# Performance work log

Measured on AMD Instinct MI355X. Metric: run time of the kernel, lower is better.

Reference implementation:

```python
import jax, jax.numpy as jnp
import numpy as np
import math

B, S, D, L, H, V, MAXP = 8, 512, 1024, 6, 8, 32000, 4096
HD = D // H
FF = 4 * D
EPS = 1e-5
SCALE = 1.0 / math.sqrt(HD)


def _ln(x, g, b):
    m = x.mean(-1, keepdims=True)
    xm = x - m
    v = (xm * xm).mean(-1, keepdims=True)
    return xm * jax.lax.rsqrt(v + EPS) * g + b


def setup_inputs() -> dict:
    key = jax.random.key(0)
    ks = jax.random.split(key, 16)
    std = 0.02
    inp = {
        'input_ids': jax.random.randint(ks[0], (B, S), 0, V, dtype=jnp.int32),
        'attention_mask': jnp.ones((B, S), dtype=jnp.int32),
        'current_position': 0,
        'tok_emb': jax.random.normal(ks[1], (V, D), jnp.float32) * std,
        'pos_emb': jax.random.normal(ks[2], (MAXP, D), jnp.float32) * std,
        'ln1_s': jnp.ones((L, D), jnp.float32),
        'ln1_b': jnp.zeros((L, D), jnp.float32),
        'Wq': jax.random.normal(ks[3], (L, D, D), jnp.float32) * std,
        'bq': jnp.zeros((L, D), jnp.float32),
        'Wk': jax.random.normal(ks[4], (L, D, D), jnp.float32) * std,
        'bk': jnp.zeros((L, D), jnp.float32),
        'Wv': jax.random.normal(ks[5], (L, D, D), jnp.float32) * std,
        'bv': jnp.zeros((L, D), jnp.float32),
        'Wo': jax.random.normal(ks[6], (L, D, D), jnp.float32) * std,
        'bo': jnp.zeros((L, D), jnp.float32),
        'ln2_s': jnp.ones((L, D), jnp.float32),
        'ln2_b': jnp.zeros((L, D), jnp.float32),
        'W1': jax.random.normal(ks[7], (L, D, FF), jnp.float32) * std,
        'b1': jnp.zeros((L, FF), jnp.float32),
        'W2': jax.random.normal(ks[8], (L, FF, D), jnp.float32) * std,
        'b2': jnp.zeros((L, D), jnp.float32),
        'lnf_s': jnp.ones((D,), jnp.float32),
        'lnf_b': jnp.zeros((D,), jnp.float32),
        'Wout': jax.random.normal(ks[9], (D, D), jnp.float32) * std,
        'bout': jnp.zeros((D,), jnp.float32),
    }
    return inp


def reference(input_ids, attention_mask, current_position, tok_emb, pos_emb,
              ln1_s, ln1_b, Wq, bq, Wk, bk, Wv, bv, Wo, bo,
              ln2_s, ln2_b, W1, b1, W2, b2, lnf_s, lnf_b, Wout, bout):
    pos = current_position + jnp.arange(S)  # [S]
    h = tok_emb[input_ids] + pos_emb[pos][None, :, :]  # [B,S,D]
    pad = (attention_mask == 0)[:, None, None, :]  # [B,1,1,S] key-padding mask

    def layer(h, p):
        (l1s, l1b, wq, bq_, wk, bk_, wv, bv_, wo, bo_,
         l2s, l2b, w1, b1_, w2, b2_) = p
        x = _ln(h, l1s, l1b)
        q = (x @ wq + bq_).reshape(B, S, H, HD).transpose(0, 2, 1, 3)
        k = (x @ wk + bk_).reshape(B, S, H, HD).transpose(0, 2, 1, 3)
        v = (x @ wv + bv_).reshape(B, S, H, HD).transpose(0, 2, 1, 3)
        scores = jnp.einsum('bhqd,bhkd->bhqk', q, k) * SCALE
        scores = jnp.where(pad, -10000.0, scores)
        attn = jax.nn.softmax(scores, axis=-1)
        o = jnp.einsum('bhqk,bhkd->bhqd', attn, v)
        o = o.transpose(0, 2, 1, 3).reshape(B, S, D)
        h = h + (o @ wo + bo_)
        x = _ln(h, l2s, l2b)
        mlp = jax.nn.gelu(x @ w1 + b1_, approximate=False) @ w2 + b2_
        return h + mlp, None

    h, _ = jax.lax.scan(layer, h, (ln1_s, ln1_b, Wq, bq, Wk, bk, Wv, bv, Wo, bo,
                                   ln2_s, ln2_b, W1, b1, W2, b2))
    h = _ln(h, lnf_s, lnf_b)
    return h @ Wout + bout
```

## Files before the change

### kernel.cpp

```cpp
#include <hip/hip_runtime.h>
#include <hip/hip_bf16.h>
#include <math.h>

#define BB 8
#define SS 512
#define DD 1024
#define LL 6
#define HH 8
#define HDD 128
#define FFF 4096
#define EPSF 1e-5f
#define SCALEF 0.08838834764831845f

typedef __attribute__((ext_vector_type(8))) _Float16 f16x8;
typedef __attribute__((ext_vector_type(4))) _Float16 f16x4;
typedef __attribute__((ext_vector_type(4))) float f32x4;

__device__ __forceinline__ void gload16(const void* g, void* l) {
  __builtin_amdgcn_global_load_lds(
      (const __attribute__((address_space(1))) void*)g,
      (__attribute__((address_space(3))) void*)l, 16, 0, 0);
}

__global__ __launch_bounds__(256, 3) void gemmk_kernel(
    const _Float16* __restrict__ Ag, const _Float16* __restrict__ Bg,
    const float* __restrict__ bias, void* __restrict__ outp,
    const int* __restrict__ amask, int Ndim, int Kdim, int Kstr,
    long zsA, long zsB, long zsOut, int emode) {
  __shared__ _Float16 lA[8192];
  __shared__ _Float16 lB[8192];
  const int tid = threadIdx.x;
  const int lane = tid & 63;
  const int wid = tid >> 6;
  const int z = blockIdx.z;
  const int m0 = blockIdx.y * 128;
  const int n0 = blockIdx.x * 128;
  const long K2 = (long)Kstr * 2;
  const _Float16* Az = Ag + (long)z * zsA + (long)m0 * Kstr;
  const _Float16* Bz = Bg + (long)z * zsB + (long)n0 * Kstr;

  const int wm = (wid >> 1) * 64;
  const int wn = (wid & 1) * 64;
  const int r16 = lane & 15;
  const int kq = lane >> 4;

  const char* As[4];
  const char* Bs[4];
  int ldd[4];
#pragma unroll
  for (int i = 0; i < 4; ++i) {
    const int idx = tid + i * 256;
    const int r = idx >> 3;
    const int sc = ((idx & 7) << 4) ^ ((r & 7) << 4);
    As[i] = (const char*)Az + (long)r * K2 + sc;
    Bs[i] = (const char*)Bz + (long)r * K2 + sc;
    ldd[i] = idx * 16;
  }
  int adA[4], adB[4];
#pragma unroll
  for (int mi = 0; mi < 4; ++mi) {
    const int R = wm + mi * 16 + r16;
    adA[mi] = R * 128 + ((kq * 16) ^ ((R & 7) << 4));
  }
#pragma unroll
  for (int ni = 0; ni < 4; ++ni) {
    const int R = wn + ni * 16 + r16;
    adB[ni] = R * 128 + ((kq * 16) ^ ((R & 7) << 4));
  }

  f32x4 acc[4][4];
#pragma unroll
  for (int mi = 0; mi < 4; ++mi)
#pragma unroll
    for (int ni = 0; ni < 4; ++ni) acc[mi][ni] = (f32x4){0.f, 0.f, 0.f, 0.f};

  const int nt = Kdim >> 6;
  for (int t = 0; t < nt; ++t) {
    const int kb = t << 7;
    __syncthreads();
#pragma unroll
    for (int i = 0; i < 4; ++i) {
      gload16(As[i] + kb, (char*)lA + ldd[i]);
      gload16(Bs[i] + kb, (char*)lB + ldd[i]);
    }
    __syncthreads();
#pragma unroll
    for (int kk = 0; kk < 2; ++kk) {
      f16x8 af[4], bf[4];
#pragma unroll
      for (int mi = 0; mi < 4; ++mi) {
        const int R = wm + mi * 16 + r16;
        af[mi] = *(const f16x8*)((const char*)lA + R * 128 +
                                 ((kk * 64 + kq * 16) ^ ((R & 7) << 4)));
      }
#pragma unroll
      for (int ni = 0; ni < 4; ++ni) {
        const int R = wn + ni * 16 + r16;
        bf[ni] = *(const f16x8*)((const char*)lB + R * 128 +
                                 ((kk * 64 + kq * 16) ^ ((R & 7) << 4)));
      }
#pragma unroll
      for (int mi = 0; mi < 4; ++mi)
#pragma unroll
        for (int ni = 0; ni < 4; ++ni)
          acc[mi][ni] = __builtin_amdgcn_mfma_f32_16x16x32_f16(
              af[mi], bf[ni], acc[mi][ni], 0, 0, 0);
    }
  }

  _Float16* outH = (_Float16*)outp + (long)z * zsOut;
  const int rj = (lane >> 4) << 2;
  const long MSZq = (long)BB * SS * DD;
#pragma unroll
  for (int mi = 0; mi < 4; ++mi) {
#pragma unroll
    for (int ni = 0; ni < 4; ++ni) {
      const int col = n0 + wn + ni * 16 + r16;
#pragma unroll
      for (int j = 0; j < 4; ++j) {
        const int row = m0 + wm + mi * 16 + rj + j;
        float vv = acc[mi][ni][j];
        if (emode == 1) {
          vv += bias[col];
          int wsel = col >> 10, c = col & 1023;
          int b_ = row >> 9, s_ = row & 511;
          int hh = c >> 7, hd_ = c & 127;
          if (wsel < 2) {
            outH[wsel * MSZq + (((long)(b_ * HH + hh)) * SS + s_) * HDD + hd_] =
                (_Float16)vv;
          } else {
            outH[2 * MSZq + (((long)(b_ * HH + hh)) * HDD + hd_) * SS + s_] =
                (_Float16)vv;
          }
        } else if (emode == 2) {
          int b_ = z >> 3;
          vv = (amask[b_ * SS + col] == 0) ? -10000.0f : vv * SCALEF;
          outH[(long)row * Ndim + col] = (_Float16)vv;
        } else if (emode == 5) {
          vv += bias[col];
          vv = 0.5f * vv * (1.0f + erff(vv * 0.70710678118654752f));
          outH[(long)row * Ndim + col] = (_Float16)vv;
        } else {
          outH[(long)row * Ndim + col] = (_Float16)vv;
        }
      }
    }
  }
}

__global__ __launch_bounds__(256) void flashpv_kernel(
    const _Float16* __restrict__ Sg, const _Float16* __restrict__ Vt,
    _Float16* __restrict__ xout) {
  const int tid = threadIdx.x;
  const int lane = tid & 63;
  const int wid = tid >> 6;
  const int bh = blockIdx.y;
  const int q0 = blockIdx.x * 128;
  const int wm = (wid >> 1) * 64;
  const int wn = (wid & 1) * 64;
  const int r16 = lane & 15;
  const int kq = lane >> 4;
  const int rj = kq << 2;
  const _Float16* Sb = Sg + (long)bh * SS * SS + (long)q0 * SS;
  const _Float16* Vb = Vt + (long)bh * HDD * SS;

  f32x4 acc[4][4];
#pragma unroll
  for (int mi = 0; mi < 4; ++mi)
#pragma unroll
    for (int ni = 0; ni < 4; ++ni) acc[mi][ni] = (f32x4){0.f, 0.f, 0.f, 0.f};
  float m[4], l[4];
#pragma unroll
  for (int mi = 0; mi < 4; ++mi) {
    m[mi] = -INFINITY;
    l[mi] = 0.f;
  }

  for (int kt = 0; kt < 4; ++kt) {
    const int kvb = kt * 128;
    f16x8 pa[4][4];
    float rf[4];
#pragma unroll
    for (int mi = 0; mi < 4; ++mi) {
      f16x8 sf[4];
#pragma unroll
      for (int ks = 0; ks < 4; ++ks)
        sf[ks] = *(const f16x8*)(Sb + (long)(wm + mi * 16 + r16) * SS + kvb +
                                 ks * 32 + kq * 8);
      float tm = -INFINITY;
#pragma unroll
      for (int ks = 0; ks < 4; ++ks)
#pragma unroll
        for (int e = 0; e < 8; ++e) tm = fmaxf(tm, (float)sf[ks][e]);
      tm = fmaxf(tm, __shfl_xor(tm, 16));
      tm = fmaxf(tm, __shfl_xor(tm, 32));
      const float mn = fmaxf(m[mi], tm);
      rf[mi] = __expf(m[mi] - mn);
      m[mi] = mn;
      float rs = 0.f;
#pragma unroll
      for (int ks = 0; ks < 4; ++ks) {
        f16x8 p;
#pragma unroll
        for (int e = 0; e < 8; ++e) {
          const float pv = __expf((float)sf[ks][e] - mn);
          rs += pv;
          p[e] = (_Float16)pv;
        }
        pa[mi][ks] = p;
      }
      rs += __shfl_xor(rs, 16);
      rs += __shfl_xor(rs, 32);
      l[mi] = l[mi] * rf[mi] + rs;
    }
#pragma unroll
    for (int mi = 0; mi < 4; ++mi)
#pragma unroll
      for (int j = 0; j < 4; ++j) {
        const float f = __shfl(rf[mi], (lane & 48) | (rj + j));
#pragma unroll
        for (int ni = 0; ni < 4; ++ni) acc[mi][ni][j] *= f;
      }
#pragma unroll
    for (int ks = 0; ks < 4; ++ks) {
      f16x8 bf[4];
#pragma unroll
      for (int ni = 0; ni < 4; ++ni)
        bf[ni] = *(const f16x8*)(Vb + (long)(wn + ni * 16 + r16) * SS + kvb +
                                 ks * 32 + kq * 8);
#pragma unroll
      for (int mi = 0; mi < 4; ++mi)
#pragma unroll
        for (int ni = 0; ni < 4; ++ni)
          acc[mi][ni] = __builtin_amdgcn_mfma_f32_16x16x32_f16(
              pa[mi][ks], bf[ni], acc[mi][ni], 0, 0, 0);
    }
  }

  float linv[4];
#pragma unroll
  for (int mi = 0; mi < 4; ++mi) linv[mi] = 1.0f / l[mi];
  const int b_ = bh >> 3, hh = bh & 7;
#pragma unroll
  for (int mi = 0; mi < 4; ++mi)
#pragma unroll
    for (int j = 0; j < 4; ++j) {
      const float f = __shfl(linv[mi], (lane & 48) | (rj + j));
      const int row = q0 + wm + mi * 16 + rj + j;
#pragma unroll
      for (int ni = 0; ni < 4; ++ni) {
        const int col = wn + ni * 16 + r16;
        xout[((long)(b_ * SS + row)) * DD + hh * HDD + col] =
            (_Float16)(acc[mi][ni][j] * f);
      }
    }
}

__global__ __launch_bounds__(256) void reduce_ln_kernel(
    const _Float16* __restrict__ parts, int npart,
    const float* __restrict__ res, const float* __restrict__ bias,
    const float* __restrict__ lg, const float* __restrict__ lb,
    float* __restrict__ hout, _Float16* __restrict__ xout, long pzs) {
  const int row = blockIdx.x;
  const int c = threadIdx.x << 2;
  const long base = (long)row * DD + c;
  float4 a = *reinterpret_cast<const float4*>(&bias[c]);
  if (res) {
    const float4 r = *reinterpret_cast<const float4*>(&res[base]);
    a.x += r.x; a.y += r.y; a.z += r.z; a.w += r.w;
  }
  for (int p = 0; p < npart; ++p) {
    const f16x4 hpv = *reinterpret_cast<const f16x4*>(&parts[p * pzs + base]);
    a.x += (float)hpv[0]; a.y += (float)hpv[1];
    a.z += (float)hpv[2]; a.w += (float)hpv[3];
  }
  *reinterpret_cast<float4*>(&hout[base]) = a;
  if (!lg) return;
  float s = a.x + a.y + a.z + a.w;
  float ss = a.x * a.x + a.y * a.y + a.z * a.z + a.w * a.w;
#pragma unroll
  for (int off = 32; off; off >>= 1) {
    s += __shfl_down(s, off);
    ss += __shfl_down(ss, off);
  }
  __shared__ float red[8];
  const int wid = threadIdx.x >> 6, lane = threadIdx.x & 63;
  if (lane == 0) { red[wid] = s; red[4 + wid] = ss; }
  __syncthreads();
  if (threadIdx.x == 0) {
    s = red[0] + red[1] + red[2] + red[3];
    ss = red[4] + red[5] + red[6] + red[7];
    float mean = s * (1.0f / DD);
    float var = ss * (1.0f / DD) - mean * mean;
    red[0] = mean;
    red[1] = rsqrtf(var + EPSF);
  }
  __syncthreads();
  const float mean = red[0], rstd = red[1];
  const float4 gv = *reinterpret_cast<const float4*>(&lg[c]);
  const float4 bv = *reinterpret_cast<const float4*>(&lb[c]);
  f16x4 o;
  o[0] = (_Float16)((a.x - mean) * rstd * gv.x + bv.x);
  o[1] = (_Float16)((a.y - mean) * rstd * gv.y + bv.y);
  o[2] = (_Float16)((a.z - mean) * rstd * gv.z + bv.z);
  o[3] = (_Float16)((a.w - mean) * rstd * gv.w + bv.w);
  *reinterpret_cast<f16x4*>(&xout[base]) = o;
}

__global__ __launch_bounds__(256) void embed_ln_kernel(
    const int* __restrict__ ids, const int* __restrict__ curpos,
    const float* __restrict__ tok, const float* __restrict__ pos,
    const float* __restrict__ lg, const float* __restrict__ lb,
    float* __restrict__ h, _Float16* __restrict__ x) {
  const int rs = blockIdx.x;
  const int s_ = rs & (SS - 1);
  const int t = ids[rs];
  const int p = curpos[0] + s_;
  const int c = threadIdx.x << 2;
  const float4 tv = *reinterpret_cast<const float4*>(&tok[(long)t * DD + c]);
  const float4 pv = *reinterpret_cast<const float4*>(&pos[(long)p * DD + c]);
  float4 a = {tv.x + pv.x, tv.y + pv.y, tv.z + pv.z, tv.w + pv.w};
  *reinterpret_cast<float4*>(&h[(long)rs * DD + c]) = a;
  float s = a.x + a.y + a.z + a.w;
  float ss = a.x * a.x + a.y * a.y + a.z * a.z + a.w * a.w;
#pragma unroll
  for (int off = 32; off; off >>= 1) {
    s += __shfl_down(s, off);
    ss += __shfl_down(ss, off);
  }
  __shared__ float red[8];
  const int wid = threadIdx.x >> 6, lane = threadIdx.x & 63;
  if (lane == 0) { red[wid] = s; red[4 + wid] = ss; }
  __syncthreads();
  if (threadIdx.x == 0) {
    s = red[0] + red[1] + red[2] + red[3];
    ss = red[4] + red[5] + red[6] + red[7];
    float mean = s * (1.0f / DD);
    float var = ss * (1.0f / DD) - mean * mean;
    red[0] = mean;
    red[1] = rsqrtf(var + EPSF);
  }
  __syncthreads();
  const float mean = red[0], rstd = red[1];
  const float4 gv = *reinterpret_cast<const float4*>(&lg[c]);
  const float4 bv = *reinterpret_cast<const float4*>(&lb[c]);
  f16x4 o;
  o[0] = (_Float16)((a.x - mean) * rstd * gv.x + bv.x);
  o[1] = (_Float16)((a.y - mean) * rstd * gv.y + bv.y);
  o[2] = (_Float16)((a.z - mean) * rstd * gv.z + bv.z);
  o[3] = (_Float16)((a.w - mean) * rstd * gv.w + bv.w);
  *reinterpret_cast<f16x4*>(&x[(long)rs * DD + c]) = o;
}

__global__ __launch_bounds__(256) void wtrans4_kernel(
    const float* __restrict__ Wq, const float* __restrict__ Wk,
    const float* __restrict__ Wv, const float* __restrict__ Wo,
    _Float16* __restrict__ qkvT, _Float16* __restrict__ woT) {
  __shared__ float t[64][65];
  const int zz = blockIdx.z;
  const float* W = (zz == 0) ? Wq : (zz == 1) ? Wk : (zz == 2) ? Wv : Wo;
  _Float16* WT = (zz < 3) ? (qkvT + (long)zz * DD * DD) : woT;
  const int n0 = blockIdx.x * 64, k0 = blockIdx.y * 64;
  const int tx = threadIdx.x & 63;
  const int ty = threadIdx.x >> 6;
#pragma unroll
  for (int i = 0; i < 16; ++i)
    t[i * 4 + ty][tx] = W[(long)(k0 + i * 4 + ty) * DD + n0 + tx];
  __syncthreads();
#pragma unroll
  for (int i = 0; i < 16; ++i) {
    const int r = i * 4 + ty;
    WT[(long)(n0 + r) * DD + k0 + tx] = (_Float16)t[tx][r];
  }
}

__global__ __launch_bounds__(256) void wtrans_kernel(
    const float* __restrict__ W, _Float16* __restrict__ WT, int K, int N) {
  __shared__ float t[64][65];
  const int n0 = blockIdx.x * 64, k0 = blockIdx.y * 64;
  const int tx = threadIdx.x & 63;
  const int ty = threadIdx.x >> 6;
#pragma unroll
  for (int i = 0; i < 16; ++i)
    t[i * 4 + ty][tx] = W[(long)(k0 + i * 4 + ty) * N + n0 + tx];
  __syncthreads();
#pragma unroll
  for (int i = 0; i < 16; ++i) {
    const int r = i * 4 + ty;
    WT[(long)(n0 + r) * K + k0 + tx] = (_Float16)t[tx][r];
  }
}

__global__ __launch_bounds__(256) void packb_kernel(
    const float* __restrict__ bq, const float* __restrict__ bk,
    const float* __restrict__ bv, float* __restrict__ bqkv) {
  const int i = blockIdx.x * 256 + threadIdx.x;
  const int l = i / (3 * DD), j = i % (3 * DD);
  float v;
  if (j < DD) v = bq[l * DD + j];
  else if (j < 2 * DD) v = bk[l * DD + j - DD];
  else v = bv[l * DD + j - 2 * DD];
  bqkv[i] = v;
}

extern "C" void kernel_launch(void* const* d_in, const int* in_sizes, int n_in,
                              void* d_out, int out_size, void* d_ws,
                              size_t ws_size, hipStream_t stream) {
  const int* ids = (const int*)d_in[0];
  const int* amask = (const int*)d_in[1];
  const int* curp = (const int*)d_in[2];
  const float* tok = (const float*)d_in[3];
  const float* pose = (const float*)d_in[4];
  const float* ln1s = (const float*)d_in[5];
  const float* ln1b = (const float*)d_in[6];
  const float* Wq = (const float*)d_in[7];
  const float* bq = (const float*)d_in[8];
  const float* Wk = (const float*)d_in[9];
  const float* bk = (const float*)d_in[10];
  const float* Wv = (const float*)d_in[11];
  const float* bv = (const float*)d_in[12];
  const float* Wo = (const float*)d_in[13];
  const float* bo = (const float*)d_in[14];
  const float* ln2s = (const float*)d_in[15];
  const float* ln2b = (const float*)d_in[16];
  const float* W1 = (const float*)d_in[17];
  const float* b1 = (const float*)d_in[18];
  const float* W2 = (const float*)d_in[19];
  const float* b2 = (const float*)d_in[20];
  const float* lnfs = (const float*)d_in[21];
  const float* lnfb = (const float*)d_in[22];
  const float* Wout = (const float*)d_in[23];
  const float* bout = (const float*)d_in[24];

  const long MSZ = (long)BB * SS * DD;
  char* wsp = (char*)d_ws;
  float* h = (float*)wsp;
  _Float16* x = (_Float16*)(wsp + 16u * 1024 * 1024);
  _Float16* q = x + MSZ;
  _Float16* kb = q + MSZ;
  _Float16* vt = kb + MSZ;
  _Float16* big = vt + MSZ;
  _Float16* wqkvT = big + (long)BB * HH * SS * SS;
  _Float16* woT = wqkvT + 3L * DD * DD;
  _Float16* w1T = woT + (long)DD * DD;
  _Float16* w2T = w1T + (long)DD * FFF;
  float* bqkv = (float*)(w2T + (long)FFF * DD);
  _Float16* parts = (_Float16*)(bqkv + LL * 3 * DD);

  const int M = BB * SS;
  dim3 blk(256);
  const long pzs = (long)M * DD;

  embed_ln_kernel<<<M, blk, 0, stream>>>(ids, curp, tok, pose, ln1s, ln1b, h, x);
  packb_kernel<<<(LL * 3 * DD) / 256, blk, 0, stream>>>(bq, bk, bv, bqkv);

  const dim3 gQKV(3 * DD / 128, M / 128, 1);
  const dim3 gS(SS / 128, SS / 128, BB * HH);
  const dim3 gPV(SS / 128, BB * HH);
  const dim3 gF1(FFF / 128, M / 128, 1);
  const dim3 gK2(DD / 128, M / 128, 2);
  const dim3 gK4(DD / 128, M / 128, 4);
  const dim3 gWt4(DD / 64, DD / 64, 4);
  const dim3 gWt(DD / 64, DD / 64);
  const dim3 gW1t(FFF / 64, DD / 64);
  const dim3 gW2t(DD / 64, FFF / 64);

  for (int l = 0; l < LL; ++l) {
    const long lo = (long)l * DD * DD;
    wtrans4_kernel<<<gWt4, blk, 0, stream>>>(Wq + lo, Wk + lo, Wv + lo, Wo + lo,
                                             wqkvT, woT);
    wtrans_kernel<<<gW1t, blk, 0, stream>>>(W1 + (long)l * DD * FFF, w1T, DD, FFF);
    wtrans_kernel<<<gW2t, blk, 0, stream>>>(W2 + (long)l * FFF * DD, w2T, FFF, DD);

    gemmk_kernel<<<gQKV, blk, 0, stream>>>(x, wqkvT, bqkv + l * 3 * DD, q,
                                           nullptr, 3 * DD, DD, DD, 0, 0, 0, 1);
    gemmk_kernel<<<gS, blk, 0, stream>>>(q, kb, nullptr, big, amask, SS, HDD,
                                         HDD, (long)SS * HDD, (long)SS * HDD,
                                         (long)SS * SS, 2);
    flashpv_kernel<<<gPV, blk, 0, stream>>>(big, vt, x);
    gemmk_kernel<<<gK2, blk, 0, stream>>>(x, woT, nullptr, parts, nullptr, DD,
                                          DD / 2, DD, DD / 2, DD / 2, pzs, 6);
    reduce_ln_kernel<<<M, blk, 0, stream>>>(parts, 2, h, bo + l * DD,
                                            ln2s + l * DD, ln2b + l * DD, h, x,
                                            pzs);
    gemmk_kernel<<<gF1, blk, 0, stream>>>(x, w1T, b1 + l * FFF, big, nullptr,
                                          FFF, DD, DD, 0, 0, 0, 5);
    gemmk_kernel<<<gK4, blk, 0, stream>>>(big, w2T, nullptr, parts, nullptr,
                                          DD, FFF / 4, FFF, FFF / 4, FFF / 4,
                                          pzs, 6);
    const float* ng = (l < LL - 1) ? (ln1s + (l + 1) * DD) : lnfs;
    const float* nb = (l < LL - 1) ? (ln1b + (l + 1) * DD) : lnfb;
    reduce_ln_kernel<<<M, blk, 0, stream>>>(parts, 4, h, b2 + l * DD, ng, nb,
                                            h, x, pzs);
  }
  wtrans_kernel<<<gWt, blk, 0, stream>>>(Wout, woT, DD, DD);
  gemmk_kernel<<<gK2, blk, 0, stream>>>(x, woT, nullptr, parts, nullptr, DD,
                                        DD / 2, DD, DD / 2, DD / 2, pzs, 6);
  reduce_ln_kernel<<<M, blk, 0, stream>>>(parts, 2, nullptr, bout, nullptr,
                                          nullptr, (float*)d_out, nullptr, pzs);
}
```

Measured before the change: 1.638 ms.

## Fuse QK^T scores into flash attention kernel and merge weight transposes

Replaces the separate score GEMM (which wrote a full BxHxSxS fp16 score matrix to global memory) and the PV kernel with a single flash-attention kernel. It computes QK^T with MFMA, applies mask and scale, runs an online softmax, stages P through shared memory and multiplies by V^T. This removes the large score-matrix round trip through HBM and one launch per layer. The three per-layer weight-transpose launches are also merged into one kernel. In exchange, each wave reloads K and V straight from global memory without LDS sharing, and the kernel adds block-level syncs.

```diff
diff --git a/kernel.cpp b/kernel.cpp
--- a/kernel.cpp
+++ b/kernel.cpp
@@ -25,8 +25,7 @@
 __global__ __launch_bounds__(256, 3) void gemmk_kernel(
     const _Float16* __restrict__ Ag, const _Float16* __restrict__ Bg,
     const float* __restrict__ bias, void* __restrict__ outp,
-    const int* __restrict__ amask, int Ndim, int Kdim, int Kstr,
-    long zsA, long zsB, long zsOut, int emode) {
+    int Ndim, int Kdim, int Kstr, long zsA, long zsB, long zsOut, int emode) {
   __shared__ _Float16 lA[8192];
   __shared__ _Float16 lB[8192];
   const int tid = threadIdx.x;
@@ -55,17 +54,6 @@
     As[i] = (const char*)Az + (long)r * K2 + sc;
     Bs[i] = (const char*)Bz + (long)r * K2 + sc;
     ldd[i] = idx * 16;
-  }
-  int adA[4], adB[4];
-#pragma unroll
-  for (int mi = 0; mi < 4; ++mi) {
-    const int R = wm + mi * 16 + r16;
-    adA[mi] = R * 128 + ((kq * 16) ^ ((R & 7) << 4));
-  }
-#pragma unroll
-  for (int ni = 0; ni < 4; ++ni) {
-    const int R = wn + ni * 16 + r16;
-    adB[ni] = R * 128 + ((kq * 16) ^ ((R & 7) << 4));
   }
 
   f32x4 acc[4][4];
@@ -132,10 +120,6 @@
             outH[2 * MSZq + (((long)(b_ * HH + hh)) * HDD + hd_) * SS + s_] =
                 (_Float16)vv;
           }
-        } else if (emode == 2) {
-          int b_ = z >> 3;
-          vv = (amask[b_ * SS + col] == 0) ? -10000.0f : vv * SCALEF;
-          outH[(long)row * Ndim + col] = (_Float16)vv;
         } else if (emode == 5) {
           vv += bias[col];
           vv = 0.5f * vv * (1.0f + erff(vv * 0.70710678118654752f));
@@ -148,111 +132,178 @@
   }
 }
 
-__global__ __launch_bounds__(256) void flashpv_kernel(
-    const _Float16* __restrict__ Sg, const _Float16* __restrict__ Vt,
+__global__ __launch_bounds__(256) void flash_kernel(
+    const _Float16* __restrict__ Qg, const _Float16* __restrict__ Kg,
+    const _Float16* __restrict__ Vt, const int* __restrict__ amask,
     _Float16* __restrict__ xout) {
+  __shared__ _Float16 Pl[4][32][136];
+  __shared__ float rf_s[4][32];
   const int tid = threadIdx.x;
   const int lane = tid & 63;
-  const int wid = tid >> 6;
+  const int w = tid >> 6;
   const int bh = blockIdx.y;
-  const int q0 = blockIdx.x * 128;
-  const int wm = (wid >> 1) * 64;
-  const int wn = (wid & 1) * 64;
+  const int b_ = bh >> 3, hh = bh & 7;
+  const int q0 = blockIdx.x * 128 + w * 32;
   const int r16 = lane & 15;
   const int kq = lane >> 4;
   const int rj = kq << 2;
-  const _Float16* Sb = Sg + (long)bh * SS * SS + (long)q0 * SS;
+  const _Float16* Qb = Qg + ((long)bh * SS + q0) * HDD;
+  const _Float16* Kb = Kg + (long)bh * SS * HDD;
   const _Float16* Vb = Vt + (long)bh * HDD * SS;
 
-  f32x4 acc[4][4];
-#pragma unroll
-  for (int mi = 0; mi < 4; ++mi)
-#pragma unroll
-    for (int ni = 0; ni < 4; ++ni) acc[mi][ni] = (f32x4){0.f, 0.f, 0.f, 0.f};
-  float m[4], l[4];
-#pragma unroll
-  for (int mi = 0; mi < 4; ++mi) {
-    m[mi] = -INFINITY;
-    l[mi] = 0.f;
-  }
+  f16x8 qa[2][4];
+#pragma unroll
+  for (int mi = 0; mi < 2; ++mi)
+#pragma unroll
+    for (int kk = 0; kk < 4; ++kk)
+      qa[mi][kk] = *(const f16x8*)(Qb + (long)(mi * 16 + r16) * HDD + kk * 32 +
+                                   kq * 8);
+
+  f32x4 acc[8][2];
+#pragma unroll
+  for (int mi = 0; mi < 8; ++mi)
+#pragma unroll
+    for (int ni = 0; ni < 2; ++ni) acc[mi][ni] = (f32x4){0.f, 0.f, 0.f, 0.f};
+  float mrun[2][4], lrun[2][4];
+#pragma unroll
+  for (int mi = 0; mi < 2; ++mi)
+#pragma unroll
+    for (int j = 0; j < 4; ++j) {
+      mrun[mi][j] = -INFINITY;
+      lrun[mi][j] = 0.f;
+    }
 
   for (int kt = 0; kt < 4; ++kt) {
-    const int kvb = kt * 128;
-    f16x8 pa[4][4];
-    float rf[4];
-#pragma unroll
-    for (int mi = 0; mi < 4; ++mi) {
-      f16x8 sf[4];
-#pragma unroll
-      for (int ks = 0; ks < 4; ++ks)
-        sf[ks] = *(const f16x8*)(Sb + (long)(wm + mi * 16 + r16) * SS + kvb +
-                                 ks * 32 + kq * 8);
-      float tm = -INFINITY;
-#pragma unroll
-      for (int ks = 0; ks < 4; ++ks)
-#pragma unroll
-        for (int e = 0; e < 8; ++e) tm = fmaxf(tm, (float)sf[ks][e]);
-      tm = fmaxf(tm, __shfl_xor(tm, 16));
-      tm = fmaxf(tm, __shfl_xor(tm, 32));
-      const float mn = fmaxf(m[mi], tm);
-      rf[mi] = __expf(m[mi] - mn);
-      m[mi] = mn;
-      float rs = 0.f;
-#pragma unroll
-      for (int ks = 0; ks < 4; ++ks) {
-        f16x8 p;
-#pragma unroll
-        for (int e = 0; e < 8; ++e) {
-          const float pv = __expf((float)sf[ks][e] - mn);
-          rs += pv;
-          p[e] = (_Float16)pv;
+    __syncthreads();
+    const int s0 = kt * 128;
+    int am[8];
+#pragma unroll
+    for (int ni = 0; ni < 8; ++ni)
+      am[ni] = amask[b_ * SS + s0 + ni * 16 + r16];
+
+    f32x4 sc[2][8];
+#pragma unroll
+    for (int mi = 0; mi < 2; ++mi)
+#pragma unroll
+      for (int ni = 0; ni < 8; ++ni) sc[mi][ni] = (f32x4){0.f, 0.f, 0.f, 0.f};
+#pragma unroll
+    for (int ni = 0; ni < 8; ++ni) {
+      f16x8 kf[4];
+#pragma unroll
+      for (int kk = 0; kk < 4; ++kk)
+        kf[kk] = *(const f16x8*)(Kb + (long)(s0 + ni * 16 + r16) * HDD +
+                                 kk * 32 + kq * 8);
+#pragma unroll
+      for (int mi = 0; mi < 2; ++mi)
+#pragma unroll
+        for (int kk = 0; kk < 4; ++kk)
+          sc[mi][ni] = __builtin_amdgcn_mfma_f32_16x16x32_f16(
+              qa[mi][kk], kf[kk], sc[mi][ni], 0, 0, 0);
+    }
+#pragma unroll
+    for (int mi = 0; mi < 2; ++mi)
+#pragma unroll
+      for (int ni = 0; ni < 8; ++ni)
+#pragma unroll
+        for (int j = 0; j < 4; ++j)
+          sc[mi][ni][j] = am[ni] ? sc[mi][ni][j] * SCALEF : -10000.0f;
+
+    float rf[2][4];
+#pragma unroll
+    for (int mi = 0; mi < 2; ++mi)
+#pragma unroll
+      for (int j = 0; j < 4; ++j) {
+        float rm = -INFINITY;
+#pragma unroll
+        for (int ni = 0; ni < 8; ++ni) rm = fmaxf(rm, sc[mi][ni][j]);
+#pragma unroll
+        for (int off = 1; off < 16; off <<= 1)
+          rm = fmaxf(rm, __shfl_xor(rm, off));
+        const float mn = fmaxf(mrun[mi][j], rm);
+        const float rfv = __expf(mrun[mi][j] - mn);
+        mrun[mi][j] = mn;
+        float rs = 0.f;
+#pragma unroll
+        for (int ni = 0; ni < 8; ++ni) {
+          const float p = __expf(sc[mi][ni][j] - mn);
+          sc[mi][ni][j] = p;
+          rs += p;
         }
-        pa[mi][ks] = p;
+#pragma unroll
+        for (int off = 1; off < 16; off <<= 1) rs += __shfl_xor(rs, off);
+        lrun[mi][j] = lrun[mi][j] * rfv + rs;
+        rf[mi][j] = rfv;
       }
-      rs += __shfl_xor(rs, 16);
-      rs += __shfl_xor(rs, 32);
-      l[mi] = l[mi] * rf[mi] + rs;
-    }
-#pragma unroll
-    for (int mi = 0; mi < 4; ++mi)
-#pragma unroll
-      for (int j = 0; j < 4; ++j) {
-        const float f = __shfl(rf[mi], (lane & 48) | (rj + j));
-#pragma unroll
-        for (int ni = 0; ni < 4; ++ni) acc[mi][ni][j] *= f;
-      }
-#pragma unroll
-    for (int ks = 0; ks < 4; ++ks) {
-      f16x8 bf[4];
-#pragma unroll
-      for (int ni = 0; ni < 4; ++ni)
-        bf[ni] = *(const f16x8*)(Vb + (long)(wn + ni * 16 + r16) * SS + kvb +
-                                 ks * 32 + kq * 8);
-#pragma unroll
-      for (int mi = 0; mi < 4; ++mi)
-#pragma unroll
-        for (int ni = 0; ni < 4; ++ni)
-          acc[mi][ni] = __builtin_amdgcn_mfma_f32_16x16x32_f16(
-              pa[mi][ks], bf[ni], acc[mi][ni], 0, 0, 0);
-    }
-  }
-
-  float linv[4];
-#pragma unroll
-  for (int mi = 0; mi < 4; ++mi) linv[mi] = 1.0f / l[mi];
-  const int b_ = bh >> 3, hh = bh & 7;
-#pragma unroll
-  for (int mi = 0; mi < 4; ++mi)
-#pragma unroll
-    for (int j = 0; j < 4; ++j) {
-      const float f = __shfl(linv[mi], (lane & 48) | (rj + j));
-      const int row = q0 + wm + mi * 16 + rj + j;
-#pragma unroll
-      for (int ni = 0; ni < 4; ++ni) {
-        const int col = wn + ni * 16 + r16;
-        xout[((long)(b_ * SS + row)) * DD + hh * HDD + col] =
-            (_Float16)(acc[mi][ni][j] * f);
-      }
+    if (r16 == 0) {
+#pragma unroll
+      for (int mi = 0; mi < 2; ++mi)
+#pragma unroll
+        for (int j = 0; j < 4; ++j) rf_s[w][mi * 16 + rj + j] = rf[mi][j];
+    }
+#pragma unroll
+    for (int mi = 0; mi < 2; ++mi)
+#pragma unroll
+      for (int ni = 0; ni < 8; ++ni)
+#pragma unroll
+        for (int j = 0; j < 4; ++j)
+          Pl[w][mi * 16 + rj + j][ni * 16 + r16] = (_Float16)sc[mi][ni][j];
+    __syncthreads();
+
+    float rfq[2];
+    rfq[0] = rf_s[w][r16];
+    rfq[1] = rf_s[w][16 + r16];
+#pragma unroll
+    for (int mi2 = 0; mi2 < 8; ++mi2)
+#pragma unroll
+      for (int ni2 = 0; ni2 < 2; ++ni2)
+#pragma unroll
+        for (int j = 0; j < 4; ++j) acc[mi2][ni2][j] *= rfq[ni2];
+
+    f16x8 pb[2][4];
+#pragma unroll
+    for (int ni2 = 0; ni2 < 2; ++ni2)
+#pragma unroll
+      for (int kk = 0; kk < 4; ++kk)
+        pb[ni2][kk] =
+            *(const f16x8*)(&Pl[w][ni2 * 16 + r16][kk * 32 + kq * 8]);
+#pragma unroll
+    for (int mi2 = 0; mi2 < 8; ++mi2) {
+      f16x8 va[4];
+#pragma unroll
+      for (int kk = 0; kk < 4; ++kk)
+        va[kk] = *(const f16x8*)(Vb + (long)(mi2 * 16 + r16) * SS + s0 +
+                                 kk * 32 + kq * 8);
+#pragma unroll
+      for (int ni2 = 0; ni2 < 2; ++ni2)
+#pragma unroll
+        for (int kk = 0; kk < 4; ++kk)
+          acc[mi2][ni2] = __builtin_amdgcn_mfma_f32_16x16x32_f16(
+              va[kk], pb[ni2][kk], acc[mi2][ni2], 0, 0, 0);
+    }
+  }
+
+  __syncthreads();
+  if (r16 == 0) {
+#pragma unroll
+    for (int mi = 0; mi < 2; ++mi)
+#pragma unroll
+      for (int j = 0; j < 4; ++j)
+        rf_s[w][mi * 16 + rj + j] = 1.0f / lrun[mi][j];
+  }
+  __syncthreads();
+  float lq[2];
+  lq[0] = rf_s[w][r16];
+  lq[1] = rf_s[w][16 + r16];
+#pragma unroll
+  for (int mi2 = 0; mi2 < 8; ++mi2)
+#pragma unroll
+    for (int ni2 = 0; ni2 < 2; ++ni2) {
+      f16x4 o;
+#pragma unroll
+      for (int j = 0; j < 4; ++j) o[j] = (_Float16)(acc[mi2][ni2][j] * lq[ni2]);
+      const int qg = q0 + ni2 * 16 + r16;
+      *(f16x4*)(&xout[((long)(b_ * SS + qg)) * DD + hh * HDD + mi2 * 16 + rj]) =
+          o;
     }
 }
 
@@ -352,42 +403,60 @@
   *reinterpret_cast<f16x4*>(&x[(long)rs * DD + c]) = o;
 }
 
-__global__ __launch_bounds__(256) void wtrans4_kernel(
+__global__ __launch_bounds__(256) void wtransall_kernel(
     const float* __restrict__ Wq, const float* __restrict__ Wk,
     const float* __restrict__ Wv, const float* __restrict__ Wo,
-    _Float16* __restrict__ qkvT, _Float16* __restrict__ woT) {
-  __shared__ float t[64][65];
-  const int zz = blockIdx.z;
-  const float* W = (zz == 0) ? Wq : (zz == 1) ? Wk : (zz == 2) ? Wv : Wo;
-  _Float16* WT = (zz < 3) ? (qkvT + (long)zz * DD * DD) : woT;
+    const float* __restrict__ W1, const float* __restrict__ W2, int l,
+    _Float16* __restrict__ qkvT, _Float16* __restrict__ woT,
+    _Float16* __restrict__ w1T, _Float16* __restrict__ w2T) {
+  __shared__ float tt[64][65];
+  const int id = blockIdx.x;
+  const float* src;
+  _Float16* dst;
+  int K, N, t;
+  const long lo = (long)l * DD * DD;
+  const long lof = (long)l * DD * FFF;
+  if (id < 1024) {
+    const int wsel = id >> 8;
+    t = id & 255;
+    src = (wsel == 0 ? Wq : wsel == 1 ? Wk : wsel == 2 ? Wv : Wo) + lo;
+    dst = (wsel < 3) ? (qkvT + (long)wsel * DD * DD) : woT;
+    K = DD; N = DD;
+  } else if (id < 2048) {
+    t = id - 1024; src = W1 + lof; dst = w1T; K = DD; N = FFF;
+  } else {
+    t = id - 2048; src = W2 + lof; dst = w2T; K = FFF; N = DD;
+  }
+  const int ntile = N >> 6;
+  const int n0 = (t % ntile) << 6;
+  const int k0 = (t / ntile) << 6;
+  const int tx = threadIdx.x & 63;
+  const int ty = threadIdx.x >> 6;
+#pragma unroll
+  for (int i = 0; i < 16; ++i)
+    tt[i * 4 + ty][tx] = src[(long)(k0 + i * 4 + ty) * N + n0 + tx];
+  __syncthreads();
+#pragma unroll
+  for (int i = 0; i < 16; ++i) {
+    const int r = i * 4 + ty;
+    dst[(long)(n0 + r) * K + k0 + tx] = (_Float16)tt[tx][r];
+  }
+}
+
+__global__ __launch_bounds__(256) void wtrans_kernel(
+    const float* __restrict__ W, _Float16* __restrict__ WT, int K, int N) {
+  __shared__ float tt[64][65];
   const int n0 = blockIdx.x * 64, k0 = blockIdx.y * 64;
   const int tx = threadIdx.x & 63;
   const int ty = threadIdx.x >> 6;
 #pragma unroll
   for (int i = 0; i < 16; ++i)
-    t[i * 4 + ty][tx] = W[(long)(k0 + i * 4 + ty) * DD + n0 + tx];
+    tt[i * 4 + ty][tx] = W[(long)(k0 + i * 4 + ty) * N + n0 + tx];
   __syncthreads();
 #pragma unroll
   for (int i = 0; i < 16; ++i) {
     const int r = i * 4 + ty;
-    WT[(long)(n0 + r) * DD + k0 + tx] = (_Float16)t[tx][r];
-  }
-}
-
-__global__ __launch_bounds__(256) void wtrans_kernel(
-    const float* __restrict__ W, _Float16* __restrict__ WT, int K, int N) {
-  __shared__ float t[64][65];
-  const int n0 = blockIdx.x * 64, k0 = blockIdx.y * 64;
-  const int tx = threadIdx.x & 63;
-  const int ty = threadIdx.x >> 6;
-#pragma unroll
-  for (int i = 0; i < 16; ++i)
-    t[i * 4 + ty][tx] = W[(long)(k0 + i * 4 + ty) * N + n0 + tx];
-  __syncthreads();
-#pragma unroll
-  for (int i = 0; i < 16; ++i) {
-    const int r = i * 4 + ty;
-    WT[(long)(n0 + r) * K + k0 + tx] = (_Float16)t[tx][r];
+    WT[(long)(n0 + r) * K + k0 + tx] = (_Float16)tt[tx][r];
   }
 }
 
@@ -455,47 +524,36 @@
   packb_kernel<<<(LL * 3 * DD) / 256, blk, 0, stream>>>(bq, bk, bv, bqkv);
 
   const dim3 gQKV(3 * DD / 128, M / 128, 1);
-  const dim3 gS(SS / 128, SS / 128, BB * HH);
-  const dim3 gPV(SS / 128, BB * HH);
+  const dim3 gFA(SS / 128, BB * HH);
   const dim3 gF1(FFF / 128, M / 128, 1);
   const dim3 gK2(DD / 128, M / 128, 2);
   const dim3 gK4(DD / 128, M / 128, 4);
-  const dim3 gWt4(DD / 64, DD / 64, 4);
   const dim3 gWt(DD / 64, DD / 64);
-  const dim3 gW1t(FFF / 64, DD / 64);
-  const dim3 gW2t(DD / 64, FFF / 64);
 
   for (int l = 0; l < LL; ++l) {
-    const long lo = (long)l * DD * DD;
-    wtrans4_kernel<<<gWt4, blk, 0, stream>>>(Wq + lo, Wk + lo, Wv + lo, Wo + lo,
-                                             wqkvT, woT);
-    wtrans_kernel<<<gW1t, blk, 0, stream>>>(W1 + (long)l * DD * FFF, w1T, DD, FFF);
-    wtrans_kernel<<<gW2t, blk, 0, stream>>>(W2 + (long)l * FFF * DD, w2T, FFF, DD);
-
+    wtransall_kernel<<<3072, blk, 0, stream>>>(Wq, Wk, Wv, Wo, W1, W2, l,
+                                               wqkvT, woT, w1T, w2T);
     gemmk_kernel<<<gQKV, blk, 0, stream>>>(x, wqkvT, bqkv + l * 3 * DD, q,
-                                           nullptr, 3 * DD, DD, DD, 0, 0, 0, 1);
-    gemmk_kernel<<<gS, blk, 0, stream>>>(q, kb, nullptr, big, amask, SS, HDD,
-                                         HDD, (long)SS * HDD, (long)SS * HDD,
-                                         (long)SS * SS, 2);
-    flashpv_kernel<<<gPV, blk, 0, stream>>>(big, vt, x);
-    gemmk_kernel<<<gK2, blk, 0, stream>>>(x, woT, nullptr, parts, nullptr, DD,
-                                          DD / 2, DD, DD / 2, DD / 2, pzs, 6);
+                                           3 * DD, DD, DD, 0, 0, 0, 1);
+    flash_kernel<<<gFA, blk, 0, stream>>>(q, kb, vt, amask, x);
+    gemmk_kernel<<<gK2, blk, 0, stream>>>(x, woT, nullptr, parts, DD, DD / 2,
+                                          DD, DD / 2, DD / 2, pzs, 6);
     reduce_ln_kernel<<<M, blk, 0, stream>>>(parts, 2, h, bo + l * DD,
                                             ln2s + l * DD, ln2b + l * DD, h, x,
                                             pzs);
-    gemmk_kernel<<<gF1, blk, 0, stream>>>(x, w1T, b1 + l * FFF, big, nullptr,
-                                          FFF, DD, DD, 0, 0, 0, 5);
-    gemmk_kernel<<<gK4, blk, 0, stream>>>(big, w2T, nullptr, parts, nullptr,
-                                          DD, FFF / 4, FFF, FFF / 4, FFF / 4,
-                                          pzs, 6);
+    gemmk_kernel<<<gF1, blk, 0, stream>>>(x, w1T, b1 + l * FFF, big, FFF, DD,
+                                          DD, 0, 0, 0, 5);
+    gemmk_kernel<<<gK4, blk, 0, stream>>>(big, w2T, nullptr, parts, DD,
+                                          FFF / 4, FFF, FFF / 4, FFF / 4, pzs,
+                                          6);
     const float* ng = (l < LL - 1) ? (ln1s + (l + 1) * DD) : lnfs;
     const float* nb = (l < LL - 1) ? (ln1b + (l + 1) * DD) : lnfb;
     reduce_ln_kernel<<<M, blk, 0, stream>>>(parts, 4, h, b2 + l * DD, ng, nb,
                                             h, x, pzs);
   }
   wtrans_kernel<<<gWt, blk, 0, stream>>>(Wout, woT, DD, DD);
-  gemmk_kernel<<<gK2, blk, 0, stream>>>(x, woT, nullptr, parts, nullptr, DD,
-                                        DD / 2, DD, DD / 2, DD / 2, pzs, 6);
+  gemmk_kernel<<<gK2, blk, 0, stream>>>(x, woT, nullptr, parts, DD, DD / 2,
+                                        DD, DD / 2, DD / 2, pzs, 6);
   reduce_ln_kernel<<<M, blk, 0, stream>>>(parts, 2, nullptr, bout, nullptr,
                                           nullptr, (float*)d_out, nullptr, pzs);
 }
```

Result: faster. 1.603 ms (-2.2%).
